# Kernel tuning notes

Measured on AMD Instinct MI355X. Metric: run time of the kernel, lower is better.

Reference implementation:

```python
import jax, jax.numpy as jnp
import numpy as np

# Physical parameter bounds in PARAM_NAMES order:
# [S1_max,S2_max,f_tens,f_rchr,f_base,r1,ku,c,alpha,psi,kappa,ki,ks,n,v,v_A,v_B,
#  Ac_max,b,lambda,chi,mu_t,T_rain,T_melt,melt_rate,lapse_rate,opg,MFMAX,MFMIN]
LOW = jnp.array([50.0,100.0,0.05,0.05,0.05,0.05,0.01,1.0,1.0,1.0,0.05,0.01,0.001,1.0,
                 0.001,0.001,0.001,0.05,0.001,5.0,2.0,0.01,-2.0,-2.0,1.0,-9.8,0.0,1.0,0.0],
                dtype=jnp.float32)
HIGH = jnp.array([5000.0,10000.0,0.95,0.95,0.95,0.95,1000.0,20.0,250.0,5.0,0.95,1000.0,
                  10000.0,10.0,0.25,0.25,0.25,0.95,3.0,10.0,5.0,5.0,4.0,4.0,10.0,0.0,1.0,10.0,10.0],
                 dtype=jnp.float32)
ROUTE_SHAPE = 2.5   # gamma routing shape (init kwarg)
KERNEL_LEN = 64     # routing kernel support (timesteps)
DT = 1.0
S1_INIT, S2_INIT = 50.0, 250.0  # state_init in the module


def _physical(raw_params):
    # low + (high-low)*sigmoid(raw), same as get_physical_params
    return LOW + (HIGH - LOW) * jax.nn.sigmoid(raw_params)


def _simulate(forcing, p):
    """Explicit-Euler 2-reservoir FUSE-style simulation. forcing: [T,3]=(prcp,pet,temp)."""
    S1_max, S2_max = p[0], p[1]
    f_tens, ku, c = p[2], p[6], p[7]
    ki, ks, n_exp = p[11], p[12], p[13]
    b, T_rain = p[18], p[22]

    def step(state, f):
        S1, S2 = state
        prcp, pet, temp = f[0], f[1], f[2]
        rain = jnp.where(temp > T_rain, prcp, 0.0)
        s1f = jnp.clip(S1 / S1_max, 0.0, 1.0)
        s2f = jnp.clip(S2 / S2_max, 0.0, 1.0)
        e1 = pet * jnp.minimum(s1f / f_tens, 1.0)          # tension-store evap
        qsx = rain * s1f ** b                               # saturation-excess runoff
        q12 = ku * s1f ** c                                 # percolation to lower store
        qif = ki * s1f                                      # interflow
        qb = ks * s2f ** n_exp                              # nonlinear baseflow
        S1n = jnp.clip(S1 + DT * (rain - qsx - e1 - q12 - qif), 0.0, S1_max)
        S2n = jnp.clip(S2 + DT * (q12 - qb), 0.0, S2_max)
        return (S1n, S2n), qsx + qif + qb

    init = (jnp.float32(S1_INIT), jnp.float32(S2_INIT))
    _, runoff = jax.lax.scan(step, init, forcing)
    return runoff  # [T]


def _route(runoff, shape, delay):
    """Causal gamma-kernel routing convolution (route_runoff)."""
    t = jnp.arange(KERNEL_LEN, dtype=jnp.float32) + 0.5
    theta = jnp.maximum(delay, 1e-3) / shape               # scale so mean = delay
    logk = (shape - 1.0) * jnp.log(t) - t / theta
    kern = jax.nn.softmax(logk)                            # normalized gamma weights
    return jnp.convolve(runoff, kern)[: runoff.shape[0]]   # causal conv


def reference(forcing, raw_params):
    phys = _physical(raw_params)
    runoff = _simulate(forcing, phys)
    # delay is used as a detached python float in the torch code -> stop_gradient
    delay = jax.lax.stop_gradient(phys[21])  # mu_t
    return _route(runoff, ROUTE_SHAPE, delay)


def setup_inputs() -> dict:
    key = jax.random.key(0)
    k1, k2, k3 = jax.random.split(key, 3)
    T = 131072
    prcp = jnp.maximum(jax.random.normal(k1, (T,)) * 5.0 + 2.0, 0.0)  # mm/day
    pet = jax.random.uniform(k2, (T,)) * 5.0                          # mm/day
    temp = jax.random.normal(k3, (T,)) * 8.0 + 5.0                    # deg C
    forcing = jnp.stack([prcp, pet, temp], axis=-1).astype(jnp.float32)
    raw_params = jnp.zeros((29,), dtype=jnp.float32)  # sigmoid(0)=0.5 -> mid-bounds
    return {"forcing": forcing, "raw_params": raw_params}
```

## Files before the change

### kernel.cpp

```cpp
#include <hip/hip_runtime.h>

#define KLEN 64
#define FCH 8
#define WARMUP 40
#define WIN_FC 64
#define WSTEP (WIN_FC * FCH)
#define RHEAD 63
#define MAXVW 8
#define S1_INIT_V 50.0f
#define S2_INIT_V 250.0f

__device__ __forceinline__ float fpow(float x, float e) {
    return exp2f(e * __log2f(x));
}
__device__ __forceinline__ float clamp01(float x) { return fminf(fmaxf(x, 0.0f), 1.0f); }
__device__ __forceinline__ float physp(const float* __restrict__ raw, int i, float lo, float hi) {
    return lo + (hi - lo) / (1.0f + __expf(-raw[i]));
}
__device__ __forceinline__ float wave_incl_scan(float x) {
#pragma unroll
    for (int o = 1; o < 64; o <<= 1) {
        float v = __shfl_up(x, o, 64);
        if ((int)threadIdx.x >= o) x += v;
    }
    return x;
}

struct F8 { float4 v[6]; };
__device__ __forceinline__ F8 load_f8(const float* __restrict__ forc, int t) {
    const float4* p = (const float4*)(forc + 3 * t);
    F8 r;
#pragma unroll
    for (int k = 0; k < 6; ++k) r.v[k] = p[k];
    return r;
}
__device__ __forceinline__ float f4c(const float4& v, int c) {
    return c == 0 ? v.x : c == 1 ? v.y : c == 2 ? v.z : v.w;
}
__device__ __forceinline__ float f8_get(const F8& f, int i) { return f4c(f.v[i >> 2], i & 3); }

#define S1_STEP(pr, pe, te, EXTRA)                                        \
    {                                                                     \
        float rain = (te) > Train ? (pr) : 0.0f;                          \
        float s1f = S1 * invS1;             \
        float lg = __log2f(s1f);                                          \
        float e1 = (pe)*fminf(s1f * invft, 1.0f);                         \
        float qsx = rain * exp2f(b * lg);                                 \
        float q12 = ku * exp2f(cc * lg);                                  \
        float qif = ki * s1f;                                             \
        EXTRA;                                                            \
        S1 = fminf(fmaxf(S1 + rain - qsx - e1 - q12 - qif, 0.0f), S1max); \
    }

__global__ void __launch_bounds__(64) k_a(
        const float* __restrict__ forc, const float* __restrict__ raw,
        float* __restrict__ q12f, float* __restrict__ Qw,
        float* __restrict__ fxg, float* __restrict__ q12g, int T, int nfine) {
    const int lane = threadIdx.x;
    const int w = blockIdx.x;
    const int j = w * WIN_FC + lane;
    const bool active = j < nfine;

    const float S1max  = physp(raw, 0, 50.0f, 5000.0f);
    const float f_tens = physp(raw, 2, 0.05f, 0.95f);
    const float ku     = physp(raw, 6, 0.01f, 1000.0f);
    const float cc     = physp(raw, 7, 1.0f, 20.0f);
    const float ki     = physp(raw, 11, 0.01f, 1000.0f);
    const float b      = physp(raw, 18, 0.001f, 3.0f);
    const float Train  = physp(raw, 22, -2.0f, 4.0f);
    const float invS1 = 1.0f / S1max, invft = 1.0f / f_tens;

    float Q = 0.0f;
    if (active) {
        const int t0 = j * FCH;
        const int tend = min(t0 + FCH, T);
        const int ts = max(t0 - WARMUP, 0);
        float S1 = S1_INIT_V;
        if (tend - t0 == FCH) {
            const int tclamp = ((T - FCH) / FCH) * FCH;
            const int ngw = (t0 - ts) >> 3;
            F8 c0 = load_f8(forc, ts);
            F8 c1 = load_f8(forc, min(ts + 8, tclamp));
            for (int g = 0; g < ngw; ++g) {
                F8 c2 = load_f8(forc, min(ts + 8 * (g + 2), tclamp));
#pragma unroll
                for (int s = 0; s < 8; ++s)
                    S1_STEP(f8_get(c0, 3 * s), f8_get(c0, 3 * s + 1), f8_get(c0, 3 * s + 2), );
                c0 = c1; c1 = c2;
            }
            float fxv[8], qv[8];
#pragma unroll
            for (int s = 0; s < 8; ++s)
                S1_STEP(f8_get(c0, 3 * s), f8_get(c0, 3 * s + 1), f8_get(c0, 3 * s + 2),
                        fxv[s] = qsx + qif; qv[s] = q12; Q += q12);
            float4* fx4 = (float4*)fxg;
            float4* q4 = (float4*)q12g;
            fx4[2 * j] = make_float4(fxv[0], fxv[1], fxv[2], fxv[3]);
            fx4[2 * j + 1] = make_float4(fxv[4], fxv[5], fxv[6], fxv[7]);
            q4[2 * j] = make_float4(qv[0], qv[1], qv[2], qv[3]);
            q4[2 * j + 1] = make_float4(qv[4], qv[5], qv[6], qv[7]);
        } else {
            for (int t = ts; t < t0; ++t) {
                float pr = forc[3 * t], pe = forc[3 * t + 1], te = forc[3 * t + 2];
                S1_STEP(pr, pe, te, );
            }
            for (int t = t0; t < tend; ++t) {
                float pr = forc[3 * t], pe = forc[3 * t + 1], te = forc[3 * t + 2];
                S1_STEP(pr, pe, te, fxg[t] = qsx + qif; q12g[t] = q12; Q += q12);
            }
        }
        q12f[j] = Q;
    }
    float s = Q;
#pragma unroll
    for (int o = 32; o >= 1; o >>= 1) s += __shfl_xor(s, o, 64);
    if (lane == 0) Qw[w] = s;
}

__global__ void __launch_bounds__(64) k_b(
        const float* __restrict__ raw, const float* __restrict__ q12f,
        const float* __restrict__ Qw, const float* __restrict__ fxg,
        const float* __restrict__ q12g, float* __restrict__ out,
        int T, int nfine, int NW) {
    __shared__ float r[RHEAD + WSTEP + 1];
    __shared__ float ldsS2[64 * MAXVW], ldsQb[64 * MAXVW];
    __shared__ float ker[KLEN];
    __shared__ float fb[2 * WIN_FC];
    const int lane = threadIdx.x;
    const int w = blockIdx.x;

    const float S2max = physp(raw, 1, 100.0f, 10000.0f);
    const float ks    = physp(raw, 12, 0.001f, 10000.0f);
    const float nn    = physp(raw, 13, 1.0f, 10.0f);
    const float invS2 = 1.0f / S2max;

    const int VW = (NW + 63) >> 6;
    bool picard_ok = (VW <= MAXVW);
    if (picard_ok) {
        float S2v[MAXVW], qbv[MAXVW], Qv[MAXVW], Lv[MAXVW];
        const float qb0 = ks * fpow(clamp01(S2_INIT_V * invS2), nn);
        for (int v = 0; v < VW; ++v) {
            int wi = lane * VW + v;
            Lv[v] = (wi < NW) ? (float)min(WSTEP, T - WSTEP * wi) : 0.0f;
            Qv[v] = (wi < NW) ? Qw[wi] : 0.0f;
            S2v[v] = S2_INIT_V; qbv[v] = qb0;
        }
        for (int it = 0; it < 12; ++it) {
            float loc[MAXVW]; float sum = 0.0f;
            for (int v = 0; v < VW; ++v) { loc[v] = sum; sum += Qv[v] - Lv[v] * qbv[v]; }
            float sc = wave_incl_scan(sum);
            float base = S2_INIT_V + (sc - sum);
            for (int v = 0; v < VW; ++v) {
                S2v[v] = base + loc[v];
                qbv[v] = ks * fpow(clamp01(S2v[v] * invS2), nn);
            }
        }
        bool bad = false;
        for (int v = 0; v < VW; ++v) {
            int wi = lane * VW + v;
            if (wi < NW)
                bad |= (S2v[v] - Lv[v] * qbv[v] < 0.5f) || (S2v[v] + Qv[v] > S2max - 0.5f) ||
                       !(S2v[v] == S2v[v]);
        }
        picard_ok = (__ballot(bad) == 0ULL);
        if (picard_ok) {
            for (int v = 0; v < VW; ++v) {
                int wi = lane * VW + v;
                if (wi < NW) { ldsS2[wi] = S2v[v]; ldsQb[wi] = qbv[v]; }
            }
        }
    }
    if (!picard_ok && lane == 0) {
        float S2 = S2_INIT_V;
        int iend = min((w + 1) * WIN_FC, nfine);
        for (int i = 0; i < iend; ++i) {
            if (w > 0 && i >= (w - 1) * WIN_FC && i < w * WIN_FC) fb[i - (w - 1) * WIN_FC] = S2;
            if (i >= w * WIN_FC) fb[WIN_FC + (i - w * WIN_FC)] = S2;
            float qbc = ks * fpow(clamp01(S2 * invS2), nn);
            float steps = (float)min(FCH, T - FCH * i);
            S2 = fminf(fmaxf(S2 + q12f[i] - steps * qbc, 0.0f), S2max);
        }
    }
    __syncthreads();

    const int j = w * WIN_FC + lane;
    const bool active = j < nfine;

    float qf = active ? q12f[j] : 0.0f;
    float sc1 = wave_incl_scan(qf);
    float S2own = 0.0f;
    if (active) {
        S2own = picard_ok
            ? fminf(fmaxf(ldsS2[w] + (sc1 - qf) - ldsQb[w] * (float)(FCH * lane), 0.0f), S2max)
            : fb[WIN_FC + lane];
    }
    float S2g = 0.0f;
    if (w > 0) {
        float qfp = q12f[(w - 1) * WIN_FC + lane];
        float sc2 = wave_incl_scan(qfp);
        S2g = picard_ok
            ? fminf(fmaxf(ldsS2[w - 1] + (sc2 - qfp) - ldsQb[w - 1] * (float)(FCH * lane), 0.0f), S2max)
            : fb[lane];
    } else if (lane < RHEAD) {
        r[lane] = 0.0f;
    }

    {
        const int base_i = FCH * lane;
        if (active) {
            const float4* fx4 = (const float4*)fxg;
            const float4* q4 = (const float4*)q12g;
            float4 fa = fx4[2 * j], fb4 = fx4[2 * j + 1];
            float4 qa = q4[2 * j], qd = q4[2 * j + 1];
            float fxv[8] = {fa.x, fa.y, fa.z, fa.w, fb4.x, fb4.y, fb4.z, fb4.w};
            float qv[8] = {qa.x, qa.y, qa.z, qa.w, qd.x, qd.y, qd.z, qd.w};
            float S2 = S2own;
            int nst = min(FCH, T - FCH * j);
#pragma unroll
            for (int s = 0; s < 8; ++s) {
                float qb = ks * fpow(clamp01(S2 * invS2), nn);
                float ro = fxv[s] + qb;
                r[RHEAD + base_i + s] = (s < nst) ? ro : 0.0f;
                S2 = fminf(fmaxf(S2 + qv[s] - qb, 0.0f), S2max);
            }
        } else {
#pragma unroll
            for (int s = 0; s < 8; ++s) r[RHEAD + base_i + s] = 0.0f;
        }
    }
    if (w > 0 && lane >= WIN_FC - 8) {
        int jg = (w - 1) * WIN_FC + lane;
        const float4* fx4 = (const float4*)fxg;
        const float4* q4 = (const float4*)q12g;
        float4 fa = fx4[2 * jg], fb4 = fx4[2 * jg + 1];
        float4 qa = q4[2 * jg], qd = q4[2 * jg + 1];
        float fxv[8] = {fa.x, fa.y, fa.z, fa.w, fb4.x, fb4.y, fb4.z, fb4.w};
        float qv[8] = {qa.x, qa.y, qa.z, qa.w, qd.x, qd.y, qd.z, qd.w};
        float S2 = S2g;
#pragma unroll
        for (int s = 0; s < 8; ++s) {
            float qb = ks * fpow(clamp01(S2 * invS2), nn);
            float ro = fxv[s] + qb;
            int p = FCH * lane + s;
            if (p >= WSTEP - RHEAD) r[p - (WSTEP - RHEAD)] = ro;
            S2 = fminf(fmaxf(S2 + qv[s] - qb, 0.0f), S2max);
        }
    }
    {
        float delay = physp(raw, 21, 0.01f, 5.0f);
        float theta = fmaxf(delay, 1e-3f) * (1.0f / 2.5f);
        float tt = (float)lane + 0.5f;
        float logk = 1.5f * __logf(tt) - tt / theta;
        float m = logk;
#pragma unroll
        for (int o = 32; o >= 1; o >>= 1) m = fmaxf(m, __shfl_xor(m, o, 64));
        float e = __expf(logk - m);
        float s = e;
#pragma unroll
        for (int o = 32; o >= 1; o >>= 1) s += __shfl_xor(s, o, 64);
        ker[lane] = e / s;
    }
    __syncthreads();

#pragma unroll 1
    for (int it = 0; it < WSTEP / 64; ++it) {
        int i = it * 64 + lane;
        int t = w * WSTEP + i;
        if (t < T) {
            float acc = 0.0f;
#pragma unroll
            for (int k = 0; k < KLEN; ++k) acc += ker[k] * r[RHEAD + i - k];
            out[t] = acc;
        }
    }
}

extern "C" void kernel_launch(void* const* d_in, const int* in_sizes, int n_in,
                              void* d_out, int out_size, void* d_ws, size_t ws_size,
                              hipStream_t stream) {
    const float* forcing = (const float*)d_in[0];
    const float* raw = (const float*)d_in[1];
    float* out = (float*)d_out;
    float* ws = (float*)d_ws;

    int T = in_sizes[0] / 3;
    int nfine = (T + FCH - 1) / FCH;
    int NW = (nfine + WIN_FC - 1) / WIN_FC;
    int P = ((nfine + 15) / 16) * 16;
    int PW = ((NW + 15) / 16) * 16;
    int Tp = P * FCH;

    float* q12f = ws;
    float* Qw = q12f + P;
    float* fxg = Qw + PW;
    float* q12g = fxg + Tp;

    k_a<<<NW, 64, 0, stream>>>(forcing, raw, q12f, Qw, fxg, q12g, T, nfine);
    k_b<<<NW, 64, 0, stream>>>(raw, q12f, Qw, fxg, q12g, out, T, nfine, NW);
}
```

Baseline: 81.62 us.

## Register-blocked routing convolution with transposed LDS layout and shuffled kernel taps

Rewrites the routing convolution so each lane computes 8 consecutive outputs. It uses a sliding register window over a transposed, bank-friendly LDS buffer and broadcasts kernel taps via shuffles instead of LDS, which cuts LDS reads per FMA and lets outputs go out as float4 stores. It also drops the clamp on the baseflow fraction and lowers the Picard iteration count from 12 to 10. The last two trim arithmetic but could change results if S2 leaves [0, S2max] or the fixed point has not converged.

Measured after the change: 77.37 us. 5.2% less time.

```diff
diff --git a/kernel.cpp b/kernel.cpp
--- a/kernel.cpp
+++ b/kernel.cpp
@@ -5,8 +5,8 @@
 #define WARMUP 40
 #define WIN_FC 64
 #define WSTEP (WIN_FC * FCH)
-#define RHEAD 63
 #define MAXVW 8
+#define ROWS 72
 #define S1_INIT_V 50.0f
 #define S2_INIT_V 250.0f
 
@@ -122,9 +122,8 @@
         const float* __restrict__ Qw, const float* __restrict__ fxg,
         const float* __restrict__ q12g, float* __restrict__ out,
         int T, int nfine, int NW) {
-    __shared__ float r[RHEAD + WSTEP + 1];
+    __shared__ float rr[8 * ROWS];
     __shared__ float ldsS2[64 * MAXVW], ldsQb[64 * MAXVW];
-    __shared__ float ker[KLEN];
     __shared__ float fb[2 * WIN_FC];
     const int lane = threadIdx.x;
     const int w = blockIdx.x;
@@ -145,7 +144,7 @@
             Qv[v] = (wi < NW) ? Qw[wi] : 0.0f;
             S2v[v] = S2_INIT_V; qbv[v] = qb0;
         }
-        for (int it = 0; it < 12; ++it) {
+        for (int it = 0; it < 10; ++it) {
             float loc[MAXVW]; float sum = 0.0f;
             for (int v = 0; v < VW; ++v) { loc[v] = sum; sum += Qv[v] - Lv[v] * qbv[v]; }
             float sc = wave_incl_scan(sum);
@@ -201,32 +200,29 @@
         S2g = picard_ok
             ? fminf(fmaxf(ldsS2[w - 1] + (sc2 - qfp) - ldsQb[w - 1] * (float)(FCH * lane), 0.0f), S2max)
             : fb[lane];
-    } else if (lane < RHEAD) {
-        r[lane] = 0.0f;
-    }
-
-    {
-        const int base_i = FCH * lane;
-        if (active) {
-            const float4* fx4 = (const float4*)fxg;
-            const float4* q4 = (const float4*)q12g;
-            float4 fa = fx4[2 * j], fb4 = fx4[2 * j + 1];
-            float4 qa = q4[2 * j], qd = q4[2 * j + 1];
-            float fxv[8] = {fa.x, fa.y, fa.z, fa.w, fb4.x, fb4.y, fb4.z, fb4.w};
-            float qv[8] = {qa.x, qa.y, qa.z, qa.w, qd.x, qd.y, qd.z, qd.w};
-            float S2 = S2own;
-            int nst = min(FCH, T - FCH * j);
-#pragma unroll
-            for (int s = 0; s < 8; ++s) {
-                float qb = ks * fpow(clamp01(S2 * invS2), nn);
-                float ro = fxv[s] + qb;
-                r[RHEAD + base_i + s] = (s < nst) ? ro : 0.0f;
-                S2 = fminf(fmaxf(S2 + qv[s] - qb, 0.0f), S2max);
-            }
-        } else {
-#pragma unroll
-            for (int s = 0; s < 8; ++s) r[RHEAD + base_i + s] = 0.0f;
-        }
+    } else {
+        rr[(lane & 7) * ROWS + (lane >> 3)] = 0.0f;
+    }
+
+    if (active) {
+        const float4* fx4 = (const float4*)fxg;
+        const float4* q4 = (const float4*)q12g;
+        float4 fa = fx4[2 * j], fb4 = fx4[2 * j + 1];
+        float4 qa = q4[2 * j], qd = q4[2 * j + 1];
+        float fxv[8] = {fa.x, fa.y, fa.z, fa.w, fb4.x, fb4.y, fb4.z, fb4.w};
+        float qv[8] = {qa.x, qa.y, qa.z, qa.w, qd.x, qd.y, qd.z, qd.w};
+        float S2 = S2own;
+        int nst = min(FCH, T - FCH * j);
+#pragma unroll
+        for (int s = 0; s < 8; ++s) {
+            float qb = ks * fpow(S2 * invS2, nn);
+            float ro = fxv[s] + qb;
+            rr[s * ROWS + lane + 8] = (s < nst) ? ro : 0.0f;
+            S2 = fminf(fmaxf(S2 + qv[s] - qb, 0.0f), S2max);
+        }
+    } else {
+#pragma unroll
+        for (int s = 0; s < 8; ++s) rr[s * ROWS + lane + 8] = 0.0f;
     }
     if (w > 0 && lane >= WIN_FC - 8) {
         int jg = (w - 1) * WIN_FC + lane;
@@ -239,13 +235,12 @@
         float S2 = S2g;
 #pragma unroll
         for (int s = 0; s < 8; ++s) {
-            float qb = ks * fpow(clamp01(S2 * invS2), nn);
-            float ro = fxv[s] + qb;
-            int p = FCH * lane + s;
-            if (p >= WSTEP - RHEAD) r[p - (WSTEP - RHEAD)] = ro;
+            float qb = ks * fpow(S2 * invS2, nn);
+            rr[s * ROWS + (lane - (WIN_FC - 8))] = fxv[s] + qb;
             S2 = fminf(fmaxf(S2 + qv[s] - qb, 0.0f), S2max);
         }
     }
+    float kreg;
     {
         float delay = physp(raw, 21, 0.01f, 5.0f);
         float theta = fmaxf(delay, 1e-3f) * (1.0f / 2.5f);
@@ -255,22 +250,41 @@
 #pragma unroll
         for (int o = 32; o >= 1; o >>= 1) m = fmaxf(m, __shfl_xor(m, o, 64));
         float e = __expf(logk - m);
-        float s = e;
-#pragma unroll
-        for (int o = 32; o >= 1; o >>= 1) s += __shfl_xor(s, o, 64);
-        ker[lane] = e / s;
+        float su = e;
+#pragma unroll
+        for (int o = 32; o >= 1; o >>= 1) su += __shfl_xor(su, o, 64);
+        kreg = e / su;
     }
     __syncthreads();
 
-#pragma unroll 1
-    for (int it = 0; it < WSTEP / 64; ++it) {
-        int i = it * 64 + lane;
-        int t = w * WSTEP + i;
-        if (t < T) {
-            float acc = 0.0f;
-#pragma unroll
-            for (int k = 0; k < KLEN; ++k) acc += ker[k] * r[RHEAD + i - k];
-            out[t] = acc;
+    {
+        float y[8];
+#pragma unroll
+        for (int s = 0; s < 8; ++s) y[s] = 0.0f;
+        float wdw[8];
+#pragma unroll
+        for (int e = 0; e < 8; ++e) {
+            int m = 8 * lane + 1 + e;
+            wdw[e] = rr[(m & 7) * ROWS + (m >> 3)];
+        }
+#pragma unroll
+        for (int jj = 0; jj < 64; ++jj) {
+            float kk = __shfl(kreg, 63 - jj, 64);
+#pragma unroll
+            for (int s = 0; s < 8; ++s) y[s] += kk * wdw[(jj + s) & 7];
+            if (jj < 63) {
+                int m = 8 * lane + 9 + jj;
+                wdw[jj & 7] = rr[(m & 7) * ROWS + (m >> 3)];
+            }
+        }
+        int tb = w * WSTEP + 8 * lane;
+        if (tb + 8 <= T) {
+            float4* op = (float4*)(out + tb);
+            op[0] = make_float4(y[0], y[1], y[2], y[3]);
+            op[1] = make_float4(y[4], y[5], y[6], y[7]);
+        } else {
+            for (int s = 0; s < 8; ++s)
+                if (tb + s < T) out[tb + s] = y[s];
         }
     }
 }
```
